# Performance work log

Measured on AMD Instinct MI355X. Metric: run time of the kernel, lower is better.

## Reference

```python
import jax, jax.numpy as jnp
import numpy as np

GROUP_SIZE = 16
MIN_SIGMA = 1e-4


def setup_inputs() -> dict:
    key = jax.random.key(0)
    k1, k2, k3 = jax.random.split(key, 3)
    B, N, M, F = 4, 8192, 4096, 64
    return {
        "point_cloud": jax.random.normal(k1, (B, 3, N), dtype=jnp.float32),
        "query_cloud": jax.random.normal(k2, (B, 3, M), dtype=jnp.float32),
        "point_features": jax.random.normal(k3, (B, F, N), dtype=jnp.float32),
        "temperature": jnp.asarray(1.0, dtype=jnp.float32),
    }


def reference(point_cloud, query_cloud, point_features, temperature):
    # point_cloud: (B,3,N), query_cloud: (B,3,M), point_features: (B,F,N)
    k = GROUP_SIZE
    # Pairwise squared distances (B, M, N): ||q||^2 + ||p||^2 - 2 q.p
    q_sq = jnp.sum(query_cloud ** 2, axis=1)              # (B, M)
    p_sq = jnp.sum(point_cloud ** 2, axis=1)              # (B, N)
    qp = jnp.einsum('bdm,bdn->bmn', query_cloud, point_cloud)
    d2 = q_sq[:, :, None] + p_sq[:, None, :] - 2.0 * qp   # (B, M, N)
    # k nearest neighbors per query
    _, idx = jax.lax.top_k(-d2, k)                         # (B, M, k)

    # Gather neighbor coords and features: (B, 3, M, k), (B, F, M, k)
    idx_b = idx[:, None, :, :]                             # (B,1,M,k)
    grouped_points = jnp.take_along_axis(
        point_cloud[:, :, None, :], jnp.broadcast_to(idx_b, (idx.shape[0], 3, idx.shape[1], k)), axis=3)
    grouped_features = jnp.take_along_axis(
        point_features[:, :, None, :],
        jnp.broadcast_to(idx_b, (idx.shape[0], point_features.shape[1], idx.shape[1], k)), axis=3)

    # Soft-projection weights
    sigma = jnp.maximum(temperature ** 2, jnp.asarray(MIN_SIGMA, dtype=temperature.dtype))
    deltas = grouped_points - query_cloud[:, :, :, None]   # (B,3,M,k)
    dist = jnp.sum(deltas ** 2, axis=1, keepdims=True) / sigma  # (B,1,M,k)
    weights = jax.nn.softmax(-dist, axis=3)                # (B,1,M,k)

    projected_points = jnp.sum(grouped_points * weights, axis=3)     # (B,3,M)
    propagated_features = jnp.sum(grouped_features * weights, axis=3)  # (B,F,M)
    return (projected_points, propagated_features)
```

## Files before the change

### kernel.cpp

```cpp
#include <hip/hip_runtime.h>


#define BB 4
#define NN 8192
#define MM 4096
#define FF 64
#define KK 16
#define CHUNK 4096
#define NCHUNK 2
#define QPW 4
#define QPB 32
#define SCAP 54
#define NTHR 1024
#define STG 33

__device__ __forceinline__ float min3f(float a, float b, float c) {
    float d;
    asm("v_min3_f32 %0, %1, %2, %3" : "=v"(d) : "v"(a), "v"(b), "v"(c));
    return d;
}

__global__ __launch_bounds__(256) void transpose_feat(const float* __restrict__ pf,
                                                      float* __restrict__ pfT) {
    __shared__ float tile[64][65];
    const int b = blockIdx.y;
    const int n0 = blockIdx.x * 64;
    const int t = threadIdx.x;
    const int n = t & 63, fq = t >> 6;
#pragma unroll
    for (int i = 0; i < 16; ++i) {
        int f = fq * 16 + i;
        tile[f][n] = pf[(size_t)b * FF * NN + (size_t)f * NN + n0 + n];
    }
    __syncthreads();
    const int f2 = t & 63, nq = t >> 6;
#pragma unroll
    for (int i = 0; i < 16; ++i) {
        int nn2 = nq * 16 + i;
        pfT[(size_t)b * NN * FF + (size_t)(n0 + nn2) * FF + f2] = tile[f2][nn2];
    }
}

__device__ __forceinline__ unsigned mapf(float f) {
    unsigned u = __float_as_uint(f);
    return (u & 0x80000000u) ? ~u : (u | 0x80000000u);
}
__device__ __forceinline__ float unmapf(unsigned k) {
    return (k & 0x80000000u) ? __uint_as_float(k ^ 0x80000000u)
                             : __uint_as_float(~k);
}

#define STAGE(C)                                                            \
    do {                                                                    \
        int base_ = (C)*CHUNK + t * 4;                                      \
        float4 x4_ = *(const float4*)(pcb + base_);                         \
        float4 y4_ = *(const float4*)(pcb + NN + base_);                    \
        float4 z4_ = *(const float4*)(pcb + 2 * NN + base_);                \
        *(float4*)(s_pts + t * 4) = x4_;                                    \
        *(float4*)(s_pts + CHUNK + t * 4) = y4_;                            \
        *(float4*)(s_pts + 2 * CHUNK + t * 4) = z4_;                        \
        float4 p4_;                                                         \
        p4_.x = fmaf(x4_.x, x4_.x, fmaf(y4_.x, y4_.x, z4_.x * z4_.x));      \
        p4_.y = fmaf(x4_.y, x4_.y, fmaf(y4_.y, y4_.y, z4_.y * z4_.y));      \
        p4_.z = fmaf(x4_.z, x4_.z, fmaf(y4_.z, y4_.z, z4_.z * z4_.z));      \
        p4_.w = fmaf(x4_.w, x4_.w, fmaf(y4_.w, y4_.w, z4_.w * z4_.w));      \
        *(float4*)(s_pts + 3 * CHUNK + t * 4) = p4_;                        \
    } while (0)

#define VAL(X, Y, Z, PS, QX, QY, QZ) \
    fmaf((X), (QX), fmaf((Y), (QY), fmaf((Z), (QZ), (PS))))

#define PUSH(WQ, V, I)                                          \
    do {                                                        \
        int pos_ = atomicAdd(&s_cnt[WQ], 1);                    \
        if (pos_ < SCAP) {                                      \
            s_surv[((WQ)*SCAP + pos_) * 2] = (V);               \
            s_surv[((WQ)*SCAP + pos_) * 2 + 1] = __int_as_float(I); \
        }                                                       \
    } while (0)

__global__ __launch_bounds__(NTHR, 8) void soft_proj_kernel(
    const float* __restrict__ pc, const float* __restrict__ qc,
    const float* __restrict__ pf, const float* __restrict__ pfT,
    const float* __restrict__ temp, float* __restrict__ out, int useT) {
    __shared__ __align__(16) float s_pts[4 * CHUNK];
    __shared__ __align__(16) float s_surv[QPB * SCAP * 2];
    __shared__ int s_cnt[QPB];
    __shared__ float s_thr[2 * QPB];
    int* s_sel = (int*)s_pts;

    const int bid = blockIdx.x;
    const int b = bid >> 7;
    const int m0 = (bid & 127) * QPB;
    const int t = threadIdx.x;
    const int wave = t >> 6;
    const int lane = t & 63;
    const int pairIdx = wave & 7;
    const int half = wave >> 3;

    const float* pcb = pc + (size_t)b * 3 * NN;
    const float* qcb = qc + (size_t)b * 3 * MM;

    float qx2[QPW], qy2[QPW], qz2[QPW];
#pragma unroll
    for (int q = 0; q < QPW; ++q) {
        int m = m0 + pairIdx * QPW + q;
        qx2[q] = -2.0f * qcb[m];
        qy2[q] = -2.0f * qcb[MM + m];
        qz2[q] = -2.0f * qcb[2 * MM + m];
    }

    float mnA[QPW], mnB[QPW];
#pragma unroll
    for (int q = 0; q < QPW; ++q) { mnA[q] = 3.0e38f; mnB[q] = 3.0e38f; }

    for (int c = 0; c < NCHUNK; ++c) {
        __syncthreads();
        STAGE(c);
        __syncthreads();
        const int ob = half * 2048 + lane * 4;
#pragma unroll
        for (int g = 0; g < 8; ++g) {
            int oo = ob + g * 256;
            float4 x4 = *(const float4*)(s_pts + oo);
            float4 y4 = *(const float4*)(s_pts + CHUNK + oo);
            float4 z4 = *(const float4*)(s_pts + 2 * CHUNK + oo);
            float4 p4 = *(const float4*)(s_pts + 3 * CHUNK + oo);
#pragma unroll
            for (int q = 0; q < QPW; ++q) {
                float v0 = VAL(x4.x, y4.x, z4.x, p4.x, qx2[q], qy2[q], qz2[q]);
                float v1 = VAL(x4.y, y4.y, z4.y, p4.y, qx2[q], qy2[q], qz2[q]);
                float v2 = VAL(x4.z, y4.z, z4.z, p4.z, qx2[q], qy2[q], qz2[q]);
                float v3 = VAL(x4.w, y4.w, z4.w, p4.w, qx2[q], qy2[q], qz2[q]);
                mnA[q] = min3f(v0, v1, mnA[q]);
                mnB[q] = min3f(v2, v3, mnB[q]);
            }
        }
    }

#pragma unroll
    for (int q = 0; q < QPW; ++q) {
        unsigned key = mapf(fminf(mnA[q], mnB[q]));
        unsigned res = 0u;
        for (int bb = 31; bb >= 16; --bb) {
            unsigned cand = res | (1u << bb);
            unsigned long long bal = __ballot(key < cand);
            int c2 = __popcll(bal);
            if (c2 < 8) res = cand;
        }
        if (lane == 0)
            s_thr[half * QPB + pairIdx * QPW + q] = unmapf(res | 0xFFFFu);
    }
    if (t < QPB) s_cnt[t] = 0;
    __syncthreads();
    float thv[QPW];
#pragma unroll
    for (int q = 0; q < QPW; ++q)
        thv[q] = fmaxf(s_thr[pairIdx * QPW + q], s_thr[QPB + pairIdx * QPW + q]);

    for (int c = 0; c < NCHUNK; ++c) {
        __syncthreads();
        STAGE(c);
        __syncthreads();
        const int ob = half * 2048 + lane * 4;
#pragma unroll
        for (int g = 0; g < 8; ++g) {
            int oo = ob + g * 256;
            float4 x4 = *(const float4*)(s_pts + oo);
            float4 y4 = *(const float4*)(s_pts + CHUNK + oo);
            float4 z4 = *(const float4*)(s_pts + 2 * CHUNK + oo);
            float4 p4 = *(const float4*)(s_pts + 3 * CHUNK + oo);
            int gi = c * CHUNK + oo;
#pragma unroll
            for (int q = 0; q < QPW; ++q) {
                float v0 = VAL(x4.x, y4.x, z4.x, p4.x, qx2[q], qy2[q], qz2[q]);
                float v1 = VAL(x4.y, y4.y, z4.y, p4.y, qx2[q], qy2[q], qz2[q]);
                float v2 = VAL(x4.z, y4.z, z4.z, p4.z, qx2[q], qy2[q], qz2[q]);
                float v3 = VAL(x4.w, y4.w, z4.w, p4.w, qx2[q], qy2[q], qz2[q]);
                if (fminf(min3f(v0, v1, v2), v3) <= thv[q]) {
                    int wqq = pairIdx * QPW + q;
                    if (v0 <= thv[q]) PUSH(wqq, v0, gi + 0);
                    if (v1 <= thv[q]) PUSH(wqq, v1, gi + 1);
                    if (v2 <= thv[q]) PUSH(wqq, v2, gi + 2);
                    if (v3 <= thv[q]) PUSH(wqq, v3, gi + 3);
                }
            }
        }
    }
    __syncthreads();

#pragma unroll
    for (int qq = 0; qq < 2; ++qq) {
        int wq = wave * 2 + qq;
        int cnt = s_cnt[wq];
        cnt = __builtin_amdgcn_readfirstlane(cnt);
        if (cnt > SCAP) cnt = SCAP;
        bool valid = lane < cnt;
        float mv = 0.f;
        int mi = 0;
        if (valid) {
            mv = s_surv[(wq * SCAP + lane) * 2];
            mi = __float_as_int(s_surv[(wq * SCAP + lane) * 2 + 1]);
        }
        int rank = 0;
        for (int j = 0; j < cnt; ++j) {
            float vj = s_surv[(wq * SCAP + j) * 2];
            int ij = __float_as_int(s_surv[(wq * SCAP + j) * 2 + 1]);
            if (valid && (vj < mv || (vj == mv && ij < mi))) rank++;
        }
        if (valid && rank < KK) s_sel[wq * KK + rank] = mi;
    }
    __syncthreads();

    float* stage = s_surv;
    float tval = temp[0];
    float sigma = fmaxf(tval * tval, 1.0e-4f);
    float inv_sigma = 1.0f / sigma;
    const float* pfTb = pfT + (size_t)b * NN * FF;
    const float* pfb = pf + (size_t)b * FF * NN;

#pragma unroll
    for (int qq = 0; qq < 2; ++qq) {
        int wq = wave * 2 + qq;
        int m = m0 + wq;
        float qxe = qcb[m], qye = qcb[MM + m], qze = qcb[2 * MM + m];
        int ik = s_sel[wq * KK + (lane & 15)];
        float px = pcb[ik], py = pcb[NN + ik], pz = pcb[2 * NN + ik];
        float dx = px - qxe, dy = py - qye, dz = pz - qze;
        float dk = fmaf(dx, dx, fmaf(dy, dy, dz * dz));
        float dmin = dk;
#pragma unroll
        for (int s = 1; s < 16; s <<= 1) dmin = fminf(dmin, __shfl_xor(dmin, s));
        float e = __expf((dmin - dk) * inv_sigma);
        float ssum = e;
#pragma unroll
        for (int s = 1; s < 16; s <<= 1) ssum += __shfl_xor(ssum, s);
        float w = e * (1.0f / ssum);
        float sx = w * px, sy = w * py, sz = w * pz;
#pragma unroll
        for (int s = 1; s < 16; s <<= 1) {
            sx += __shfl_xor(sx, s);
            sy += __shfl_xor(sy, s);
            sz += __shfl_xor(sz, s);
        }
        float facc = 0.f;
#pragma unroll
        for (int k = 0; k < KK; ++k) {
            float wk = __shfl(w, k);
            int iik = __shfl(ik, k);
            float fv = useT ? pfTb[(size_t)iik * FF + lane]
                            : pfb[(size_t)lane * NN + iik];
            facc = fmaf(wk, fv, facc);
        }
        stage[lane * STG + wq] = facc;
        if (lane == 0) {
            stage[(64) * STG + wq] = sx;
            stage[(65) * STG + wq] = sy;
            stage[(66) * STG + wq] = sz;
        }
    }
    __syncthreads();

    const size_t featOff = (size_t)BB * 3 * MM;
    for (int j = t; j < 67 * QPB; j += NTHR) {
        int row = j >> 5, col = j & 31;
        float v = stage[row * STG + col];
        int m = m0 + col;
        if (row < 64)
            out[featOff + (size_t)b * FF * MM + (size_t)row * MM + m] = v;
        else
            out[(size_t)b * 3 * MM + (size_t)(row - 64) * MM + m] = v;
    }
}

extern "C" void kernel_launch(void* const* d_in, const int* in_sizes, int n_in,
                              void* d_out, int out_size, void* d_ws, size_t ws_size,
                              hipStream_t stream) {
    (void)in_sizes; (void)n_in; (void)out_size;
    const float* pc = (const float*)d_in[0];
    const float* qc = (const float*)d_in[1];
    const float* pf = (const float*)d_in[2];
    const float* temp = (const float*)d_in[3];
    float* out = (float*)d_out;
    float* pfT = (float*)d_ws;
    const size_t needT = (size_t)BB * NN * FF * sizeof(float);
    int useT = (ws_size >= needT && d_ws != nullptr) ? 1 : 0;

    if (useT) {
        hipLaunchKernelGGL(transpose_feat, dim3(NN / 64, BB), dim3(256), 0, stream,
                           pf, pfT);
    }
    hipLaunchKernelGGL(soft_proj_kernel, dim3((BB * MM) / QPB), dim3(NTHR), 0,
                       stream, pc, qc, pf, pfT, temp, out, useT);
}
```

Before: 119.3 us.

## Rescan only candidate lanes in second pass and pad point LDS layout

The second distance pass no longer recomputes every point for every query. Each lane's minimum from the first pass is compared against the threshold and ballotted into a mask. Only lanes whose 32 points can hold survivors are revisited, packing up to 8 such lanes across the wave's 64 threads per iteration. The shared point arrays also get padding every 256 floats, meant to reduce LDS bank conflicts on the strided float4 reads. The cost is extra bit-scan and select logic and a slightly larger shared buffer.

```diff
diff --git a/kernel.cpp b/kernel.cpp
--- a/kernel.cpp
+++ b/kernel.cpp
@@ -7,6 +7,7 @@
 #define FF 64
 #define KK 16
 #define CHUNK 4096
+#define PCH 4160
 #define NCHUNK 2
 #define QPW 4
 #define QPB 32
@@ -53,18 +54,19 @@
 #define STAGE(C)                                                            \
     do {                                                                    \
         int base_ = (C)*CHUNK + t * 4;                                      \
+        int pad_ = t * 4 + (t >> 6) * 4;                                    \
         float4 x4_ = *(const float4*)(pcb + base_);                         \
         float4 y4_ = *(const float4*)(pcb + NN + base_);                    \
         float4 z4_ = *(const float4*)(pcb + 2 * NN + base_);                \
-        *(float4*)(s_pts + t * 4) = x4_;                                    \
-        *(float4*)(s_pts + CHUNK + t * 4) = y4_;                            \
-        *(float4*)(s_pts + 2 * CHUNK + t * 4) = z4_;                        \
+        *(float4*)(s_pts + pad_) = x4_;                                     \
+        *(float4*)(s_pts + PCH + pad_) = y4_;                               \
+        *(float4*)(s_pts + 2 * PCH + pad_) = z4_;                           \
         float4 p4_;                                                         \
         p4_.x = fmaf(x4_.x, x4_.x, fmaf(y4_.x, y4_.x, z4_.x * z4_.x));      \
         p4_.y = fmaf(x4_.y, x4_.y, fmaf(y4_.y, y4_.y, z4_.y * z4_.y));      \
         p4_.z = fmaf(x4_.z, x4_.z, fmaf(y4_.z, y4_.z, z4_.z * z4_.z));      \
         p4_.w = fmaf(x4_.w, x4_.w, fmaf(y4_.w, y4_.w, z4_.w * z4_.w));      \
-        *(float4*)(s_pts + 3 * CHUNK + t * 4) = p4_;                        \
+        *(float4*)(s_pts + 3 * PCH + pad_) = p4_;                           \
     } while (0)
 
 #define VAL(X, Y, Z, PS, QX, QY, QZ) \
@@ -83,7 +85,7 @@
     const float* __restrict__ pc, const float* __restrict__ qc,
     const float* __restrict__ pf, const float* __restrict__ pfT,
     const float* __restrict__ temp, float* __restrict__ out, int useT) {
-    __shared__ __align__(16) float s_pts[4 * CHUNK];
+    __shared__ __align__(16) float s_pts[4 * PCH];
     __shared__ __align__(16) float s_surv[QPB * SCAP * 2];
     __shared__ int s_cnt[QPB];
     __shared__ float s_thr[2 * QPB];
@@ -118,14 +120,14 @@
         __syncthreads();
         STAGE(c);
         __syncthreads();
-        const int ob = half * 2048 + lane * 4;
+        const int obp = half * 2080 + lane * 4;
 #pragma unroll
         for (int g = 0; g < 8; ++g) {
-            int oo = ob + g * 256;
+            int oo = obp + g * 260;
             float4 x4 = *(const float4*)(s_pts + oo);
-            float4 y4 = *(const float4*)(s_pts + CHUNK + oo);
-            float4 z4 = *(const float4*)(s_pts + 2 * CHUNK + oo);
-            float4 p4 = *(const float4*)(s_pts + 3 * CHUNK + oo);
+            float4 y4 = *(const float4*)(s_pts + PCH + oo);
+            float4 z4 = *(const float4*)(s_pts + 2 * PCH + oo);
+            float4 p4 = *(const float4*)(s_pts + 3 * PCH + oo);
 #pragma unroll
             for (int q = 0; q < QPW; ++q) {
                 float v0 = VAL(x4.x, y4.x, z4.x, p4.x, qx2[q], qy2[q], qz2[q]);
@@ -137,10 +139,13 @@
             }
         }
     }
+    float mnq[QPW];
+#pragma unroll
+    for (int q = 0; q < QPW; ++q) mnq[q] = fminf(mnA[q], mnB[q]);
 
 #pragma unroll
     for (int q = 0; q < QPW; ++q) {
-        unsigned key = mapf(fminf(mnA[q], mnB[q]));
+        unsigned key = mapf(mnq[q]);
         unsigned res = 0u;
         for (int bb = 31; bb >= 16; --bb) {
             unsigned cand = res | (1u << bb);
@@ -158,26 +163,50 @@
     for (int q = 0; q < QPW; ++q)
         thv[q] = fmaxf(s_thr[pairIdx * QPW + q], s_thr[QPB + pairIdx * QPW + q]);
 
+    unsigned long long umq[QPW];
+#pragma unroll
+    for (int q = 0; q < QPW; ++q) umq[q] = __ballot(mnq[q] <= thv[q]);
+
     for (int c = 0; c < NCHUNK; ++c) {
         __syncthreads();
         STAGE(c);
         __syncthreads();
-        const int ob = half * 2048 + lane * 4;
-#pragma unroll
-        for (int g = 0; g < 8; ++g) {
-            int oo = ob + g * 256;
-            float4 x4 = *(const float4*)(s_pts + oo);
-            float4 y4 = *(const float4*)(s_pts + CHUNK + oo);
-            float4 z4 = *(const float4*)(s_pts + 2 * CHUNK + oo);
-            float4 p4 = *(const float4*)(s_pts + 3 * CHUNK + oo);
-            int gi = c * CHUNK + oo;
-#pragma unroll
-            for (int q = 0; q < QPW; ++q) {
+#pragma unroll
+        for (int q = 0; q < QPW; ++q) {
+            unsigned long long um = umq[q];
+            while (um) {
+                unsigned long long u = um;
+                int L0 = __ffsll(u) - 1; u &= u - 1;
+                int L1 = __ffsll(u) - 1; u &= u - 1;
+                int L2 = __ffsll(u) - 1; u &= u - 1;
+                int L3 = __ffsll(u) - 1; u &= u - 1;
+                int L4 = __ffsll(u) - 1; u &= u - 1;
+                int L5 = __ffsll(u) - 1; u &= u - 1;
+                int L6 = __ffsll(u) - 1; u &= u - 1;
+                int L7 = __ffsll(u) - 1; u &= u - 1;
+                int np = __popcll(um);
+                if (np > 8) np = 8;
+                um = u;
+                int myit = lane >> 3;
+                int La = (myit & 2) ? ((myit & 1) ? L3 : L2)
+                                    : ((myit & 1) ? L1 : L0);
+                int Lb = (myit & 2) ? ((myit & 1) ? L7 : L6)
+                                    : ((myit & 1) ? L5 : L4);
+                int L = (myit & 4) ? Lb : La;
+                bool act = myit < np;
+                L = act ? L : 0;
+                int g = lane & 7;
+                int ap = half * 2080 + L * 4 + g * 260;
+                float4 x4 = *(const float4*)(s_pts + ap);
+                float4 y4 = *(const float4*)(s_pts + PCH + ap);
+                float4 z4 = *(const float4*)(s_pts + 2 * PCH + ap);
+                float4 p4 = *(const float4*)(s_pts + 3 * PCH + ap);
                 float v0 = VAL(x4.x, y4.x, z4.x, p4.x, qx2[q], qy2[q], qz2[q]);
                 float v1 = VAL(x4.y, y4.y, z4.y, p4.y, qx2[q], qy2[q], qz2[q]);
                 float v2 = VAL(x4.z, y4.z, z4.z, p4.z, qx2[q], qy2[q], qz2[q]);
                 float v3 = VAL(x4.w, y4.w, z4.w, p4.w, qx2[q], qy2[q], qz2[q]);
-                if (fminf(min3f(v0, v1, v2), v3) <= thv[q]) {
+                if (act && fminf(min3f(v0, v1, v2), v3) <= thv[q]) {
+                    int gi = c * CHUNK + half * 2048 + L * 4 + g * 256;
                     int wqq = pairIdx * QPW + q;
                     if (v0 <= thv[q]) PUSH(wqq, v0, gi + 0);
                     if (v1 <= thv[q]) PUSH(wqq, v1, gi + 1);
```

Result: no change. 120.7 us (+1.2%).
